# Kernel optimization log

Hardware: AMD Instinct MI355X
Metric: run time of the kernel (lower is better)

## Reference

```python
import jax, jax.numpy as jnp
import numpy as np

B, C, W, H = 4, 256, 64, 64
AC = C // 4  # attn channels


def setup_inputs() -> dict:
    key = jax.random.key(0)
    ks = jax.random.split(key, 4)
    x = jax.random.normal(ks[0], (B, C, W, H), dtype=jnp.float32)
    Wq = jax.random.normal(ks[1], (AC, C), dtype=jnp.float32) * (1.0 / np.sqrt(C))
    Wk = jax.random.normal(ks[2], (AC, C), dtype=jnp.float32) * (1.0 / np.sqrt(C))
    Wv = jax.random.normal(ks[3], (C, C), dtype=jnp.float32) * (1.0 / np.sqrt(C))
    bq = jnp.zeros((AC,), dtype=jnp.float32)
    bk = jnp.zeros((AC,), dtype=jnp.float32)
    bv = jnp.zeros((C,), dtype=jnp.float32)
    gamma = jnp.zeros((1,), dtype=jnp.float32)
    return {"x": x, "Wq": Wq, "bq": bq, "Wk": Wk, "bk": bk, "Wv": Wv, "bv": bv, "gamma": gamma}


def reference(x, Wq, bq, Wk, bk, Wv, bv, gamma):
    b, c, w, h = x.shape
    n = w * h
    xf = x.reshape(b, c, n)  # [B, C, N]
    # 1x1 convs == channel GEMMs
    q = jnp.einsum('oc,bcn->bon', Wq, xf) + bq[None, :, None]  # [B, AC, N]
    k = jnp.einsum('oc,bcn->bon', Wk, xf) + bk[None, :, None]  # [B, AC, N]
    v = jnp.einsum('oc,bcn->bon', Wv, xf) + bv[None, :, None]  # [B, C, N]
    # attn[b, i, j] = sum_c q[b, c, i] * k[b, c, j]  (query transposed)
    attn = jnp.einsum('bci,bcj->bij', q, k)  # [B, N, N]
    # NOTE: non-standard softmax over dim=1 (over query index i for each column j)
    attn = jax.nn.softmax(attn, axis=1)
    # attn_out = attn @ value.T  -> [B, N, C]
    attn_out = jnp.einsum('bij,bcj->bic', attn, v)
    attn_out = attn_out.reshape(b, w, h, c).transpose(0, 3, 1, 2)  # [B, C, W, H]
    return gamma[0] * attn_out + x
```

## Files before the change

kernel.cpp:

```cpp
#include <hip/hip_runtime.h>
#include <hip/hip_bf16.h>

#define BB 4
#define CC 256
#define NN 4096
#define AC2 64
#define PP 72
#define JT 32
#define LOG2E 1.4426950408889634f

typedef __attribute__((ext_vector_type(4))) float f32x4;
typedef __attribute__((ext_vector_type(8))) short bf16x8;

__device__ __forceinline__ short f2bf(float f) {
    unsigned u = __builtin_bit_cast(unsigned, f);
    u = u + 0x7FFFu + ((u >> 16) & 1u);
    return (short)(u >> 16);
}
__device__ __forceinline__ float bf2f(unsigned short h) {
    unsigned u = ((unsigned)h) << 16;
    return __builtin_bit_cast(float, u);
}

__global__ __launch_bounds__(256) void prep_kernel(
    const float* __restrict__ Wq, const float* __restrict__ Wk,
    const float* __restrict__ Wv, short* __restrict__ Wb)
{
    const int idx = (blockIdx.x * 256 + threadIdx.x) * 4;
    const int o = idx >> 8, c = idx & 255;
    const float* row = (o < 64) ? (Wq + o * CC)
                     : (o < 128) ? (Wk + (o - 64) * CC)
                                 : (Wv + (o - 128) * CC);
    float4 v = *(const float4*)&row[c];
    short4 s4;
    s4.x = f2bf(v.x); s4.y = f2bf(v.y); s4.z = f2bf(v.z); s4.w = f2bf(v.w);
    *(short4*)&Wb[idx] = s4;
}

__global__ __launch_bounds__(512) void qkv_kernel(
    const float* __restrict__ x, const short* __restrict__ Wb,
    const float* __restrict__ bq, const float* __restrict__ bk,
    const float* __restrict__ bv,
    short* __restrict__ Qt, short* __restrict__ Kt, short* __restrict__ V)
{
    __shared__ __align__(16) short Xl[32 * 72];
    const int bid0 = blockIdx.x;
    const int xcd = bid0 & 7;
    const int b = xcd >> 1, nh = xcd & 1;
    const int n0 = (nh * 64 + (bid0 >> 3)) << 5;
    const int tid = threadIdx.x;
    const int lane = tid & 63, w = tid >> 6;
    const int l15 = lane & 15, lh = lane >> 4;

    f32x4 acc[3][2];
#pragma unroll
    for (int i = 0; i < 3; ++i)
#pragma unroll
        for (int j = 0; j < 2; ++j) acc[i][j] = (f32x4){0.f, 0.f, 0.f, 0.f};

    for (int ck = 0; ck < 4; ++ck) {
        const int c0 = ck << 6;
        bf16x8 Af[3][2];
#pragma unroll
        for (int of = 0; of < 3; ++of)
#pragma unroll
            for (int ks = 0; ks < 2; ++ks)
                Af[of][ks] = *(const bf16x8*)&Wb[(size_t)(w * 48 + of * 16 + l15) * CC +
                                                 c0 + ks * 32 + (lh << 3)];
        {
            const int cr = tid >> 3, q4 = tid & 7;
            float4 v = *(const float4*)&x[((size_t)(b * CC + c0 + cr)) * NN + n0 + q4 * 4];
            Xl[(q4 * 4 + 0) * 72 + cr] = f2bf(v.x);
            Xl[(q4 * 4 + 1) * 72 + cr] = f2bf(v.y);
            Xl[(q4 * 4 + 2) * 72 + cr] = f2bf(v.z);
            Xl[(q4 * 4 + 3) * 72 + cr] = f2bf(v.w);
        }
        __syncthreads();
#pragma unroll
        for (int ks = 0; ks < 2; ++ks) {
            const int co = ks * 32 + (lh << 3);
            bf16x8 Bf[2];
#pragma unroll
            for (int nf = 0; nf < 2; ++nf)
                Bf[nf] = *(const bf16x8*)&Xl[(nf * 16 + l15) * 72 + co];
#pragma unroll
            for (int of = 0; of < 3; ++of)
#pragma unroll
                for (int nf = 0; nf < 2; ++nf)
                    acc[of][nf] = __builtin_amdgcn_mfma_f32_16x16x32_bf16(
                        Af[of][ks], Bf[nf], acc[of][nf], 0, 0, 0);
        }
        __syncthreads();
    }
#pragma unroll
    for (int of = 0; of < 3; ++of) {
        const int obase = w * 48 + of * 16 + (lh << 2);
        float bias[4];
#pragma unroll
        for (int r = 0; r < 4; ++r) {
            int o = obase + r;
            bias[r] = (o < 64) ? bq[o] : (o < 128) ? bk[o - 64] : bv[o - 128];
        }
#pragma unroll
        for (int nf = 0; nf < 2; ++nf) {
            const int n = n0 + nf * 16 + l15;
            if (obase < 64) {
                short4 pk;
                pk.x = f2bf((acc[of][nf][0] + bias[0]) * LOG2E);
                pk.y = f2bf((acc[of][nf][1] + bias[1]) * LOG2E);
                pk.z = f2bf((acc[of][nf][2] + bias[2]) * LOG2E);
                pk.w = f2bf((acc[of][nf][3] + bias[3]) * LOG2E);
                *(short4*)(Qt + ((size_t)b * NN + n) * AC2 + obase) = pk;
            } else if (obase < 128) {
                short4 pk;
                pk.x = f2bf(acc[of][nf][0] + bias[0]);
                pk.y = f2bf(acc[of][nf][1] + bias[1]);
                pk.z = f2bf(acc[of][nf][2] + bias[2]);
                pk.w = f2bf(acc[of][nf][3] + bias[3]);
                *(short4*)(Kt + ((size_t)b * NN + n) * AC2 + (obase - 64)) = pk;
            } else {
#pragma unroll
                for (int r = 0; r < 4; ++r) {
                    int o = obase + r - 128;
                    V[(((size_t)b * CC + o) * NN) + n] = f2bf(acc[of][nf][r] + bias[r]);
                }
            }
        }
    }
}

__global__ __launch_bounds__(256) void stats_kernel(
    const short* __restrict__ Qt, const short* __restrict__ Kt,
    float* __restrict__ tArr)
{
    const int bid0 = blockIdx.x;
    const int xcd = bid0 & 7;
    const int b = xcd >> 1;
    const int j0 = (((xcd & 1) << 7) | (bid0 >> 3)) << 4;
    const int tid = threadIdx.x;
    const int lane = tid & 63, w = tid >> 6;
    const int l15 = lane & 15, lh = lane >> 4;
    const short* Qb = Qt + (size_t)b * NN * AC2;

    bf16x8 Bf[2];
#pragma unroll
    for (int ks = 0; ks < 2; ++ks)
        Bf[ks] = *(const bf16x8*)&Kt[((size_t)b * NN + j0 + l15) * AC2 +
                                     ks * 32 + (lh << 3)];

    bf16x8 A0[4], A1[4];
#pragma unroll
    for (int f = 0; f < 4; ++f) {
        const size_t rowA = (size_t)(w * 1024 + f * 16 + l15);
        A0[f] = *(const bf16x8*)&Qb[rowA * AC2 + (lh << 3)];
        A1[f] = *(const bf16x8*)&Qb[rowA * AC2 + 32 + (lh << 3)];
    }

    float m_run = -INFINITY, l_run = 0.f;
    for (int ii = 0; ii < 16; ++ii) {
        bf16x8 A0n[4], A1n[4];
        const int in0 = w * 1024 + ((ii + 1) & 15) * 64;
#pragma unroll
        for (int f = 0; f < 4; ++f) {
            const size_t rowA = (size_t)(in0 + f * 16 + l15);
            A0n[f] = *(const bf16x8*)&Qb[rowA * AC2 + (lh << 3)];
            A1n[f] = *(const bf16x8*)&Qb[rowA * AC2 + 32 + (lh << 3)];
        }
        f32x4 s[4];
#pragma unroll
        for (int f = 0; f < 4; ++f) {
            f32x4 t = (f32x4){0.f, 0.f, 0.f, 0.f};
            t = __builtin_amdgcn_mfma_f32_16x16x32_bf16(A0[f], Bf[0], t, 0, 0, 0);
            t = __builtin_amdgcn_mfma_f32_16x16x32_bf16(A1[f], Bf[1], t, 0, 0, 0);
            s[f] = t;
        }
        float mx = s[0][0];
#pragma unroll
        for (int f = 0; f < 4; ++f)
#pragma unroll
            for (int r = 0; r < 4; ++r) mx = fmaxf(mx, s[f][r]);
        const float m_new = fmaxf(m_run, mx);
        float add = 0.f;
#pragma unroll
        for (int f = 0; f < 4; ++f)
#pragma unroll
            for (int r = 0; r < 4; ++r) add += exp2f(s[f][r] - m_new);
        l_run = l_run * exp2f(m_run - m_new) + add;
        m_run = m_new;
#pragma unroll
        for (int f = 0; f < 4; ++f) { A0[f] = A0n[f]; A1[f] = A1n[f]; }
    }
#pragma unroll
    for (int off = 16; off <= 32; off <<= 1) {
        float m2 = __shfl_xor(m_run, off);
        float l2 = __shfl_xor(l_run, off);
        float mm = fmaxf(m_run, m2);
        l_run = l_run * exp2f(m_run - mm) + l2 * exp2f(m2 - mm);
        m_run = mm;
    }
    __shared__ float sm[4][16];
    __shared__ float sl[4][16];
    if (lane < 16) { sm[w][lane] = m_run; sl[w][lane] = l_run; }
    __syncthreads();
    if (tid < 16) {
        float m = sm[0][tid], l = sl[0][tid];
#pragma unroll
        for (int q = 1; q < 4; ++q) {
            float m2 = sm[q][tid], l2 = sl[q][tid];
            float mm = fmaxf(m, m2);
            l = l * exp2f(m - mm) + l2 * exp2f(m2 - mm);
            m = mm;
        }
        tArr[(size_t)b * NN + j0 + tid] = m + log2f(l);
    }
}

template<int ABL>
__global__ __launch_bounds__(256, 4) void out_core(
    const short* __restrict__ Qt, const short* __restrict__ Kt,
    const short* __restrict__ V,
    const float* __restrict__ tArr,
    float* __restrict__ out)
{
    __shared__ __align__(16) short Kl[2][64 * PP];
    __shared__ __align__(16) short Pl[2][64 * PP];
    const int bid0 = blockIdx.x;
    const int xcd = bid0 & 7;
    const int b = xcd >> 1, jh = xcd & 1;
    const int slot = bid0 >> 3;
    const int itile = slot >> 1, cs = slot & 1;
    const int i0 = itile << 6, c0 = cs << 7;
    const int jbase = jh << 11;
    const int tid = threadIdx.x;
    const int lane = tid & 63, w = tid >> 6;
    const int l15 = lane & 15, lh = lane >> 4;
    const int iw = i0 + (w << 4);

    const short* Ktb = Kt + (size_t)b * NN * AC2;
    const float* tb  = tArr + (size_t)b * NN + jbase;
    const short* Vb  = V + ((size_t)(b * CC + c0 + (w << 5))) * NN + jbase;

    const int krow = tid >> 2, kch = (tid & 3) << 4;
    const short* Ksrc = Ktb + ((size_t)(jbase + krow)) * AC2 + kch;
    short* const KlwA = &Kl[0][krow * PP + kch];
    short* const KlwB = &Kl[1][krow * PP + kch];

    bf16x8 Aq[2];
#pragma unroll
    for (int ks = 0; ks < 2; ++ks)
        Aq[ks] = *(const bf16x8*)&Qt[((size_t)b * NN + iw + l15) * AC2 +
                                     ks * 32 + (lh << 3)];

    f32x4 acc[2][4];
#pragma unroll
    for (int cf = 0; cf < 2; ++cf)
#pragma unroll
        for (int f = 0; f < 4; ++f) acc[cf][f] = (f32x4){0.f, 0.f, 0.f, 0.f};

    {
        bf16x8 k0a = *(const bf16x8*)(Ksrc + 0);
        bf16x8 k0b = *(const bf16x8*)(Ksrc + 8);
        *(bf16x8*)(KlwA + 0) = k0a;
        *(bf16x8*)(KlwA + 8) = k0b;
    }
    bf16x8 KpA = *(const bf16x8*)(Ksrc + (1 << 12));
    bf16x8 KpB = *(const bf16x8*)(Ksrc + (1 << 12) + 8);
    bf16x8 Vc[2][2];
#pragma unroll
    for (int cf = 0; cf < 2; ++cf)
#pragma unroll
        for (int ks = 0; ks < 2; ++ks)
            Vc[cf][ks] = *(const bf16x8*)&Vb[(size_t)(cf * 16 + l15) * NN +
                                             ks * 32 + (lh << 3)];
    f32x4 Tc4[4];
    if constexpr (ABL == 0) {
#pragma unroll
        for (int jf = 0; jf < 4; ++jf)
            Tc4[jf] = *(const f32x4*)&tb[jf * 16 + (lh << 2)];
    }
    asm volatile("s_waitcnt lgkmcnt(0)" ::: "memory");
    __builtin_amdgcn_s_barrier();
    asm volatile("" ::: "memory");

    for (int jt = 0; jt < JT; ++jt) {
        const int cur = jt & 1;
        {
            short* kd = cur ? KlwA : KlwB;
            *(bf16x8*)(kd + 0) = KpA;
            *(bf16x8*)(kd + 8) = KpB;
        }
        {
            const size_t t2 = (size_t)((jt + 2) & (JT - 1)) << 12;
            KpA = *(const bf16x8*)(Ksrc + t2);
            KpB = *(const bf16x8*)(Ksrc + t2 + 8);
        }
        bf16x8 Vn[2][2];
        f32x4 Tn4[4];
        {
            const int tv = ((jt + 1) & (JT - 1)) << 6;
#pragma unroll
            for (int cf = 0; cf < 2; ++cf)
#pragma unroll
                for (int ks = 0; ks < 2; ++ks)
                    Vn[cf][ks] = *(const bf16x8*)&Vb[(size_t)(cf * 16 + l15) * NN +
                                                     tv + ks * 32 + (lh << 3)];
            if constexpr (ABL == 0) {
#pragma unroll
                for (int jf = 0; jf < 4; ++jf)
                    Tn4[jf] = *(const f32x4*)&tb[tv + jf * 16 + (lh << 2)];
            }
        }
        short* Pw = &Pl[cur][0];
#pragma unroll
        for (int jf = 0; jf < 4; ++jf) {
            bf16x8 Ka = *(const bf16x8*)&Kl[cur][(jf * 16 + l15) * PP + (lh << 3)];
            bf16x8 Kb = *(const bf16x8*)&Kl[cur][(jf * 16 + l15) * PP + 32 + (lh << 3)];
            f32x4 s = (f32x4){0.f, 0.f, 0.f, 0.f};
            s = __builtin_amdgcn_mfma_f32_16x16x32_bf16(Ka, Aq[0], s, 0, 0, 0);
            s = __builtin_amdgcn_mfma_f32_16x16x32_bf16(Kb, Aq[1], s, 0, 0, 0);
            if constexpr (ABL == 0) {
                float e0 = exp2f(s[0] - Tc4[jf][0]);
                float e1 = exp2f(s[1] - Tc4[jf][1]);
                float e2 = exp2f(s[2] - Tc4[jf][2]);
                float e3 = exp2f(s[3] - Tc4[jf][3]);
                unsigned p01, p23;
                asm volatile("v_cvt_pk_bf16_f32 %0, %1, %2"
                             : "=v"(p01) : "v"(e0), "v"(e1));
                asm volatile("v_cvt_pk_bf16_f32 %0, %1, %2"
                             : "=v"(p23) : "v"(e2), "v"(e3));
                uint2 pk; pk.x = p01; pk.y = p23;
                *(uint2*)&Pw[(w * 16 + l15) * PP + jf * 16 + (lh << 2)] = pk;
            } else {
                asm volatile("" :: "v"(s[0]), "v"(s[1]), "v"(s[2]), "v"(s[3]));
            }
        }
        asm volatile("s_waitcnt lgkmcnt(0)" ::: "memory");
        __builtin_amdgcn_s_barrier();
        asm volatile("" ::: "memory");
#pragma unroll
        for (int ks = 0; ks < 2; ++ks) {
#pragma unroll
            for (int f = 0; f < 4; ++f) {
                bf16x8 Bp = *(const bf16x8*)&Pw[(f * 16 + l15) * PP +
                                                ks * 32 + (lh << 3)];
#pragma unroll
                for (int cf = 0; cf < 2; ++cf)
                    acc[cf][f] = __builtin_amdgcn_mfma_f32_16x16x32_bf16(
                        Vc[cf][ks], Bp, acc[cf][f], 0, 0, 0);
            }
        }
#pragma unroll
        for (int cf = 0; cf < 2; ++cf) {
            Vc[cf][0] = Vn[cf][0]; Vc[cf][1] = Vn[cf][1];
        }
        if constexpr (ABL == 0) {
#pragma unroll
            for (int jf = 0; jf < 4; ++jf) Tc4[jf] = Tn4[jf];
        }
    }

    if constexpr (ABL == 0) {
        unsigned short* po = (unsigned short*)out;
#pragma unroll
        for (int cf = 0; cf < 2; ++cf) {
#pragma unroll
            for (int r = 0; r < 4; ++r) {
                const int c = c0 + (w << 5) + cf * 16 + (lh << 2) + r;
#pragma unroll
                for (int f = 0; f < 4; ++f) {
                    const size_t gi = ((size_t)(b * CC + c)) * NN + i0 + f * 16 + l15;
                    po[gi * 2 + jh] = (unsigned short)f2bf(acc[cf][f][r]);
                }
            }
        }
    } else {
        float sink = 0.f;
#pragma unroll
        for (int cf = 0; cf < 2; ++cf)
#pragma unroll
            for (int f = 0; f < 4; ++f)
#pragma unroll
                for (int r = 0; r < 4; ++r) sink += acc[cf][f][r];
        asm volatile("" :: "v"(sink));
    }
}

__global__ __launch_bounds__(256) void reduce_kernel(
    const float* __restrict__ x, const float* __restrict__ gamma,
    float* __restrict__ out)
{
    const float g = gamma[0];
    const size_t total = (size_t)BB * CC * NN / 4;
    for (size_t i = (size_t)blockIdx.x * 256 + threadIdx.x; i < total;
         i += (size_t)2048 * 256) {
        uint4 pv = ((const uint4*)out)[i];
        float4 xv = ((const float4*)x)[i];
        float4 o;
        o.x = g * (bf2f(pv.x & 0xFFFFu) + bf2f(pv.x >> 16)) + xv.x;
        o.y = g * (bf2f(pv.y & 0xFFFFu) + bf2f(pv.y >> 16)) + xv.y;
        o.z = g * (bf2f(pv.z & 0xFFFFu) + bf2f(pv.z >> 16)) + xv.z;
        o.w = g * (bf2f(pv.w & 0xFFFFu) + bf2f(pv.w >> 16)) + xv.w;
        ((float4*)out)[i] = o;
    }
}

extern "C" void kernel_launch(void* const* d_in, const int* in_sizes, int n_in,
                              void* d_out, int out_size, void* d_ws, size_t ws_size,
                              hipStream_t stream) {
    const float* x     = (const float*)d_in[0];
    const float* Wq    = (const float*)d_in[1];
    const float* bq    = (const float*)d_in[2];
    const float* Wk    = (const float*)d_in[3];
    const float* bk    = (const float*)d_in[4];
    const float* Wv    = (const float*)d_in[5];
    const float* bv    = (const float*)d_in[6];
    const float* gamma = (const float*)d_in[7];
    float* out = (float*)d_out;

    short* Qt = (short*)d_ws;
    short* Kt = Qt + (size_t)BB * NN * AC2;
    short* V  = Kt + (size_t)BB * NN * AC2;
    float* tArr = (float*)(V + (size_t)BB * CC * NN);
    short* Wb = (short*)(tArr + (size_t)BB * NN);

    prep_kernel<<<96, 256, 0, stream>>>(Wq, Wk, Wv, Wb);
    qkv_kernel<<<BB * 128, 512, 0, stream>>>(x, Wb, bq, bk, bv, Qt, Kt, V);
    stats_kernel<<<BB * 256, 256, 0, stream>>>(Qt, Kt, tArr);
    out_core<0><<<BB * 256, 256, 0, stream>>>(Qt, Kt, V, tArr, out);
    reduce_kernel<<<2048, 256, 0, stream>>>(x, gamma, out);
    out_core<1><<<BB * 256, 256, 0, stream>>>(Qt, Kt, V, tArr, out);
}
```

Before: 359.0 us.

## Drop ablation launch, load V/T in place, raise MFMA priority, pad LDS

Removes the templated ablation variant and its extra out_core<1> launch, which did redundant work after the reduce. Inside the loop, V and T tiles are now loaded right where they are used instead of being register-prefetched one iteration ahead. This cuts register pressure but can expose global-load latency. It also raises wave priority around the PV MFMA block with s_setprio and changes the LDS row pitch from 72 to 76 to alter bank mapping.

```diff
diff --git a/kernel.cpp b/kernel.cpp
--- a/kernel.cpp
+++ b/kernel.cpp
@@ -5,7 +5,7 @@
 #define CC 256
 #define NN 4096
 #define AC2 64
-#define PP 72
+#define PP 76
 #define JT 32
 #define LOG2E 1.4426950408889634f
 
@@ -215,7 +215,6 @@
     }
 }
 
-template<int ABL>
 __global__ __launch_bounds__(256, 4) void out_core(
     const short* __restrict__ Qt, const short* __restrict__ Kt,
     const short* __restrict__ V,
@@ -265,25 +264,13 @@
     }
     bf16x8 KpA = *(const bf16x8*)(Ksrc + (1 << 12));
     bf16x8 KpB = *(const bf16x8*)(Ksrc + (1 << 12) + 8);
-    bf16x8 Vc[2][2];
-#pragma unroll
-    for (int cf = 0; cf < 2; ++cf)
-#pragma unroll
-        for (int ks = 0; ks < 2; ++ks)
-            Vc[cf][ks] = *(const bf16x8*)&Vb[(size_t)(cf * 16 + l15) * NN +
-                                             ks * 32 + (lh << 3)];
-    f32x4 Tc4[4];
-    if constexpr (ABL == 0) {
-#pragma unroll
-        for (int jf = 0; jf < 4; ++jf)
-            Tc4[jf] = *(const f32x4*)&tb[jf * 16 + (lh << 2)];
-    }
     asm volatile("s_waitcnt lgkmcnt(0)" ::: "memory");
     __builtin_amdgcn_s_barrier();
     asm volatile("" ::: "memory");
 
     for (int jt = 0; jt < JT; ++jt) {
         const int cur = jt & 1;
+        const int jb = jt << 6;
         {
             short* kd = cur ? KlwA : KlwB;
             *(bf16x8*)(kd + 0) = KpA;
@@ -294,51 +281,38 @@
             KpA = *(const bf16x8*)(Ksrc + t2);
             KpB = *(const bf16x8*)(Ksrc + t2 + 8);
         }
-        bf16x8 Vn[2][2];
-        f32x4 Tn4[4];
-        {
-            const int tv = ((jt + 1) & (JT - 1)) << 6;
-#pragma unroll
-            for (int cf = 0; cf < 2; ++cf)
-#pragma unroll
-                for (int ks = 0; ks < 2; ++ks)
-                    Vn[cf][ks] = *(const bf16x8*)&Vb[(size_t)(cf * 16 + l15) * NN +
-                                                     tv + ks * 32 + (lh << 3)];
-            if constexpr (ABL == 0) {
-#pragma unroll
-                for (int jf = 0; jf < 4; ++jf)
-                    Tn4[jf] = *(const f32x4*)&tb[tv + jf * 16 + (lh << 2)];
-            }
-        }
         short* Pw = &Pl[cur][0];
 #pragma unroll
         for (int jf = 0; jf < 4; ++jf) {
             bf16x8 Ka = *(const bf16x8*)&Kl[cur][(jf * 16 + l15) * PP + (lh << 3)];
             bf16x8 Kb = *(const bf16x8*)&Kl[cur][(jf * 16 + l15) * PP + 32 + (lh << 3)];
+            f32x4 tj = *(const f32x4*)&tb[jb + jf * 16 + (lh << 2)];
             f32x4 s = (f32x4){0.f, 0.f, 0.f, 0.f};
             s = __builtin_amdgcn_mfma_f32_16x16x32_bf16(Ka, Aq[0], s, 0, 0, 0);
             s = __builtin_amdgcn_mfma_f32_16x16x32_bf16(Kb, Aq[1], s, 0, 0, 0);
-            if constexpr (ABL == 0) {
-                float e0 = exp2f(s[0] - Tc4[jf][0]);
-                float e1 = exp2f(s[1] - Tc4[jf][1]);
-                float e2 = exp2f(s[2] - Tc4[jf][2]);
-                float e3 = exp2f(s[3] - Tc4[jf][3]);
-                unsigned p01, p23;
-                asm volatile("v_cvt_pk_bf16_f32 %0, %1, %2"
-                             : "=v"(p01) : "v"(e0), "v"(e1));
-                asm volatile("v_cvt_pk_bf16_f32 %0, %1, %2"
-                             : "=v"(p23) : "v"(e2), "v"(e3));
-                uint2 pk; pk.x = p01; pk.y = p23;
-                *(uint2*)&Pw[(w * 16 + l15) * PP + jf * 16 + (lh << 2)] = pk;
-            } else {
-                asm volatile("" :: "v"(s[0]), "v"(s[1]), "v"(s[2]), "v"(s[3]));
-            }
+            float e0 = exp2f(s[0] - tj[0]);
+            float e1 = exp2f(s[1] - tj[1]);
+            float e2 = exp2f(s[2] - tj[2]);
+            float e3 = exp2f(s[3] - tj[3]);
+            unsigned p01, p23;
+            asm volatile("v_cvt_pk_bf16_f32 %0, %1, %2"
+                         : "=v"(p01) : "v"(e0), "v"(e1));
+            asm volatile("v_cvt_pk_bf16_f32 %0, %1, %2"
+                         : "=v"(p23) : "v"(e2), "v"(e3));
+            uint2 pk; pk.x = p01; pk.y = p23;
+            *(uint2*)&Pw[(w * 16 + l15) * PP + jf * 16 + (lh << 2)] = pk;
         }
         asm volatile("s_waitcnt lgkmcnt(0)" ::: "memory");
         __builtin_amdgcn_s_barrier();
         asm volatile("" ::: "memory");
+        __builtin_amdgcn_s_setprio(1);
 #pragma unroll
         for (int ks = 0; ks < 2; ++ks) {
+            bf16x8 Vc[2];
+#pragma unroll
+            for (int cf = 0; cf < 2; ++cf)
+                Vc[cf] = *(const bf16x8*)&Vb[(size_t)(cf * 16 + l15) * NN +
+                                             jb + ks * 32 + (lh << 3)];
 #pragma unroll
             for (int f = 0; f < 4; ++f) {
                 bf16x8 Bp = *(const bf16x8*)&Pw[(f * 16 + l15) * PP +
@@ -346,42 +320,24 @@
 #pragma unroll
                 for (int cf = 0; cf < 2; ++cf)
                     acc[cf][f] = __builtin_amdgcn_mfma_f32_16x16x32_bf16(
-                        Vc[cf][ks], Bp, acc[cf][f], 0, 0, 0);
+                        Vc[cf], Bp, acc[cf][f], 0, 0, 0);
             }
         }
-#pragma unroll
-        for (int cf = 0; cf < 2; ++cf) {
-            Vc[cf][0] = Vn[cf][0]; Vc[cf][1] = Vn[cf][1];
-        }
-        if constexpr (ABL == 0) {
-#pragma unroll
-            for (int jf = 0; jf < 4; ++jf) Tc4[jf] = Tn4[jf];
-        }
-    }
-
-    if constexpr (ABL == 0) {
-        unsigned short* po = (unsigned short*)out;
-#pragma unroll
-        for (int cf = 0; cf < 2; ++cf) {
-#pragma unroll
-            for (int r = 0; r < 4; ++r) {
-                const int c = c0 + (w << 5) + cf * 16 + (lh << 2) + r;
-#pragma unroll
-                for (int f = 0; f < 4; ++f) {
-                    const size_t gi = ((size_t)(b * CC + c)) * NN + i0 + f * 16 + l15;
-                    po[gi * 2 + jh] = (unsigned short)f2bf(acc[cf][f][r]);
-                }
+        __builtin_amdgcn_s_setprio(0);
+    }
+
+    unsigned short* po = (unsigned short*)out;
+#pragma unroll
+    for (int cf = 0; cf < 2; ++cf) {
+#pragma unroll
+        for (int r = 0; r < 4; ++r) {
+            const int c = c0 + (w << 5) + cf * 16 + (lh << 2) + r;
+#pragma unroll
+            for (int f = 0; f < 4; ++f) {
+                const size_t gi = ((size_t)(b * CC + c)) * NN + i0 + f * 16 + l15;
+                po[gi * 2 + jh] = (unsigned short)f2bf(acc[cf][f][r]);
             }
         }
-    } else {
-        float sink = 0.f;
-#pragma unroll
-        for (int cf = 0; cf < 2; ++cf)
-#pragma unroll
-            for (int f = 0; f < 4; ++f)
-#pragma unroll
-                for (int r = 0; r < 4; ++r) sink += acc[cf][f][r];
-        asm volatile("" :: "v"(sink));
     }
 }
 
@@ -426,7 +382,6 @@
     prep_kernel<<<96, 256, 0, stream>>>(Wq, Wk, Wv, Wb);
     qkv_kernel<<<BB * 128, 512, 0, stream>>>(x, Wb, bq, bk, bv, Qt, Kt, V);
     stats_kernel<<<BB * 256, 256, 0, stream>>>(Qt, Kt, tArr);
-    out_core<0><<<BB * 256, 256, 0, stream>>>(Qt, Kt, V, tArr, out);
+    out_core<<<BB * 256, 256, 0, stream>>>(Qt, Kt, V, tArr, out);
     reduce_kernel<<<2048, 256, 0, stream>>>(x, gamma, out);
-    out_core<1><<<BB * 256, 256, 0, stream>>>(Qt, Kt, V, tArr, out);
-}
+}
```

New measurement: 343.0 us. -4.4%, faster.
